# Performance work log

Measured on AMD Instinct MI355X. Metric: run time of the kernel, lower is better.

Reference implementation:

```python
import jax, jax.numpy as jnp
import numpy as np
from jax import ops as jops

N = 20000          # nodes
E = 320000         # edges
IN_DIM = 16        # input_dim_features_extractor
HID = 64           # hidden_dim_features_extractor
HEADS = 4          # n_attention_heads
LAYERS = 2         # n_layers_features_extractor
NEG_SLOPE = 0.2    # DGL EGATConv leaky_relu slope


def setup_inputs() -> dict:
    key = jax.random.key(0)
    ks = jax.random.split(key, 16)
    s = lambda *sh: 1.0 / np.sqrt(sh[-2] if len(sh) >= 2 else sh[-1])
    inp = {
        "node_feat": jax.random.normal(ks[0], (N, IN_DIM), jnp.float32),
        "edge_feat": jax.random.normal(ks[1], (E, HID), jnp.float32),
        "src": jax.random.randint(ks[2], (E,), 0, N, jnp.int32),
        "dst": jax.random.randint(ks[3], (E,), 0, N, jnp.int32),
        # features_embedder (MLP n_layers=1 -> single Linear IN_DIM->HID)
        "W_embed": jax.random.normal(ks[4], (IN_DIM, HID), jnp.float32) * s(IN_DIM, HID),
        "b_embed": jnp.zeros((HID,), jnp.float32),
        # per-layer EGATConv params (stacked over layer dim)
        "W_ni": jax.random.normal(ks[5], (LAYERS, HID, HEADS * HID), jnp.float32) * s(HID, 1),
        "W_nj": jax.random.normal(ks[6], (LAYERS, HID, HEADS * HID), jnp.float32) * s(HID, 1),
        "W_fij": jax.random.normal(ks[7], (LAYERS, HID, HEADS * HID), jnp.float32) * s(HID, 1),
        "b_att": jnp.zeros((LAYERS, HEADS * HID), jnp.float32),
        "attn": jax.random.normal(ks[8], (LAYERS, HEADS, HID), jnp.float32) * s(HID),
        "W_node": jax.random.normal(ks[9], (LAYERS, HID, HEADS * HID), jnp.float32) * s(HID, 1),
        # per-layer MLP (n_layers=1 -> Linear HEADS*HID -> HID)
        "W_mlp": jax.random.normal(ks[10], (LAYERS, HEADS * HID, HID), jnp.float32) * s(HEADS * HID, 1),
        "b_mlp": jnp.zeros((LAYERS, HID), jnp.float32),
    }
    return inp


def _egat(h, f, src, dst, W_ni, W_nj, W_fij, b, attn, W_node):
    """DGL EGATConv: edge-feature attention + softmax-weighted aggregation."""
    # per-edge attention features: u_add_v + edge proj + bias
    f_ni = h @ W_ni                         # (N, H*D)
    f_nj = h @ W_nj                         # (N, H*D)
    f_fij = f @ W_fij                       # (E, H*D)
    f_out = f_ni[src] + f_nj[dst] + f_fij + b
    f_out = jax.nn.leaky_relu(f_out, NEG_SLOPE).reshape(E, HEADS, HID)
    e = jnp.einsum("ehd,hd->eh", f_out, attn)            # (E, H) logits
    # edge softmax over incoming edges of each dst node (numerically stable)
    m = jops.segment_max(e, dst, num_segments=N)          # (N, H)
    a = jnp.exp(e - m[dst])
    z = jops.segment_sum(a, dst, num_segments=N)          # (N, H)
    a = a / z[dst]
    # weighted message aggregation
    hn = (h @ W_node).reshape(N, HEADS, HID)
    msg = hn[src] * a[:, :, None]                         # (E, H, D)
    out = jops.segment_sum(msg, dst, num_segments=N)      # (N, H, D)
    return out


def reference(node_feat, edge_feat, src, dst, W_embed, b_embed,
              W_ni, W_nj, W_fij, b_att, attn, W_node, W_mlp, b_mlp):
    features_list = [node_feat]                 # layer_pooling='all'
    features = node_feat @ W_embed + b_embed    # features_embedder
    features_list.append(features)
    for L in range(LAYERS):
        h = _egat(features, edge_feat, src, dst,
                  W_ni[L], W_nj[L], W_fij[L], b_att[L], attn[L], W_node[L])
        new = h.reshape(N, HEADS * HID) @ W_mlp[L] + b_mlp[L]
        features = new + features               # residual
        features_list.append(features)
    return jnp.concatenate(features_list, axis=-1)   # (N, 16 + 3*64)
```

## Files before the change

kernel.cpp:

```cpp
#include <hip/hip_runtime.h>
#include <math.h>

#define NN 20000
#define NE 320000
#define IN_DIM 16
#define HID 64
#define HEADS 4
#define HD 256
#define OUTW 208
#define NEG 0.2f

typedef unsigned short u16;
typedef unsigned int u32;
typedef __attribute__((ext_vector_type(8))) short bf16x8;
typedef __attribute__((ext_vector_type(8))) unsigned short u16x8;
typedef __attribute__((ext_vector_type(4))) float f32x4;

__device__ __forceinline__ float b2f(u16 u) {
  union { u32 i; float f; } c; c.i = ((u32)u) << 16; return c.f;
}
__device__ __forceinline__ u16 f2b(float f) {
  union { float f; u32 i; } c; c.f = f;
  u32 r = (c.i + 0x7FFFu + ((c.i >> 16) & 1u)) >> 16;
  return (u16)r;
}

__global__ void k_embed_count(const float* __restrict__ nf, const float* __restrict__ We,
                              const float* __restrict__ be, float* __restrict__ feat,
                              float* __restrict__ out, const int* __restrict__ dst,
                              int* __restrict__ counts) {
  int bid = blockIdx.x;
  const int EB = (NN * 64) / 256;
  if (bid < EB) {
    int tid = bid * 256 + threadIdx.x;
    int n = tid >> 6, c = tid & 63;
    float acc = be[c];
#pragma unroll
    for (int k = 0; k < IN_DIM; ++k)
      acc += nf[n * IN_DIM + k] * We[k * HID + c];
    feat[n * HID + c] = acc;
    out[n * OUTW + 16 + c] = acc;
    if (c < IN_DIM) out[n * OUTW + c] = nf[n * IN_DIM + c];
  } else {
    int e = (bid - EB) * 256 + threadIdx.x;
    if (e < NE) atomicAdd(&counts[dst[e]], 1);
  }
}

__global__ void k_scan(const int* __restrict__ counts, int* __restrict__ rowptr,
                       int* __restrict__ cursor) {
  __shared__ int wsum[16];
  const int PT = 20;
  int t = threadIdx.x;
  int lane = t & 63, wid = t >> 6;
  int base = t * PT;
  int c[PT];
  int tot = 0;
  if (t < 1000) {
#pragma unroll
    for (int i = 0; i < PT; ++i) {
      int v = counts[base + i];
      cursor[base + i] = 0;
      tot += v;
      c[i] = tot;
    }
  }
  int x = tot;
#pragma unroll
  for (int d = 1; d < 64; d <<= 1) {
    int y = __shfl_up(x, d);
    if (lane >= d) x += y;
  }
  int lexcl = x - tot;
  if (lane == 63) wsum[wid] = x;
  __syncthreads();
  if (wid == 0) {
    int wv = (lane < 16) ? wsum[lane] : 0;
#pragma unroll
    for (int d = 1; d < 16; d <<= 1) {
      int y = __shfl_up(wv, d);
      if (lane >= d) wv += y;
    }
    if (lane < 16) wsum[lane] = wv;
  }
  __syncthreads();
  int woff = (wid == 0) ? 0 : wsum[wid - 1];
  int offset = woff + lexcl;
  if (t == 0) rowptr[0] = 0;
  if (t < 1000) {
#pragma unroll
    for (int i = 0; i < PT; ++i) rowptr[base + i + 1] = offset + c[i];
  }
}

__global__ void k_scatter(const int* __restrict__ dst, const int* __restrict__ src,
                          const int* __restrict__ rowptr, int* __restrict__ cursor,
                          int* __restrict__ srcp, int* __restrict__ dstp,
                          int* __restrict__ pos_of) {
  int e = blockIdx.x * blockDim.x + threadIdx.x;
  if (e >= NE) return;
  int d = dst[e];
  int pos = rowptr[d] + atomicAdd(&cursor[d], 1);
  srcp[pos] = src[e];
  dstp[pos] = d;
  pos_of[e] = pos;
}

__global__ void k_permute_prepw(const float* __restrict__ ef, const int* __restrict__ pos_of,
                                u16* __restrict__ efbp, const float* __restrict__ Wf,
                                u16* __restrict__ Wt0, u16* __restrict__ Wt1) {
  int bid = blockIdx.x;
  const int PB = (NE * 16) / 256;
  if (bid < PB) {
    int t = bid * 256 + threadIdx.x;
    int e = t >> 4, c = (t & 15) * 4;
    int slot = pos_of[e];
    float4 v = *reinterpret_cast<const float4*>(&ef[(size_t)e * HID + c]);
    ushort4 o;
    o.x = f2b(v.x); o.y = f2b(v.y); o.z = f2b(v.z); o.w = f2b(v.w);
    *reinterpret_cast<ushort4*>(&efbp[(size_t)slot * HID + c]) = o;
  } else {
    int r = (bid - PB) * 256 + threadIdx.x;
    int Lw = r >> 14;
    int idx = r & 16383;
    int nn2 = idx >> 6, kk2 = idx & 63;
    u16* WtL = Lw ? Wt1 : Wt0;
    WtL[nn2 * HID + kk2] = f2b(Wf[(size_t)Lw * HID * HD + kk2 * HD + nn2]);
  }
}

__global__ __launch_bounds__(256) void k_nodeproj(
    const float* __restrict__ feat, const float* __restrict__ Wni,
    const float* __restrict__ Wnj, const float* __restrict__ Wnd,
    const float* __restrict__ batt, u16* __restrict__ fni,
    u16* __restrict__ fnj, u16* __restrict__ hn) {
  __shared__ float hs[8 * HID];
  int n0 = blockIdx.x * 8;
  int c = threadIdx.x;
  for (int i = threadIdx.x; i < 8 * HID; i += 256)
    hs[i] = feat[(size_t)(n0 + (i >> 6)) * HID + (i & 63)];
  __syncthreads();
  float aI[8] = {0}, aJ[8] = {0}, aN[8] = {0};
  for (int k = 0; k < HID; ++k) {
    float wi = Wni[k * HD + c], wj = Wnj[k * HD + c], wn = Wnd[k * HD + c];
#pragma unroll
    for (int t = 0; t < 8; ++t) {
      float x = hs[t * HID + k];
      aI[t] += x * wi; aJ[t] += x * wj; aN[t] += x * wn;
    }
  }
  float b = batt[c];
#pragma unroll
  for (int t = 0; t < 8; ++t) {
    int n = n0 + t;
    fni[(size_t)n * HD + c] = f2b(aI[t] + b);
    fnj[(size_t)n * HD + c] = f2b(aJ[t]);
    hn[(size_t)n * HD + c]  = f2b(aN[t]);
  }
}

__global__ __launch_bounds__(256) void k_edgelogits(
    const u16* __restrict__ efbp, const int* __restrict__ srcp,
    const int* __restrict__ dstp, const u16* __restrict__ fni,
    const u16* __restrict__ fnj, const u16* __restrict__ Wt,
    const float* __restrict__ attnL, float* __restrict__ elog) {
  __shared__ float gb[HEADS][16][68];
  int h = threadIdx.x >> 6;
  int l = threadIdx.x & 63;
  int q = l >> 4;
  int n = l & 15;
  bf16x8 bfr[4][2];
#pragma unroll
  for (int nt = 0; nt < 4; ++nt)
#pragma unroll
    for (int kk = 0; kk < 2; ++kk)
      bfr[nt][kk] = *reinterpret_cast<const bf16x8*>(
          &Wt[(h * 64 + nt * 16 + n) * HID + kk * 32 + q * 8]);
  float at[4];
#pragma unroll
  for (int nt = 0; nt < 4; ++nt) at[nt] = attnL[h * 64 + nt * 16 + n];

#define COMMIT(av, bv)                                                \
  {                                                                   \
    _Pragma("unroll")                                                 \
    for (int p = 0; p < 4; ++p) {                                     \
      float4 g;                                                       \
      g.x = b2f(av[p].x) + b2f(bv[p].x);                              \
      g.y = b2f(av[p].y) + b2f(bv[p].y);                              \
      g.z = b2f(av[p].z) + b2f(bv[p].z);                              \
      g.w = b2f(av[p].w) + b2f(bv[p].w);                              \
      *reinterpret_cast<float4*>(&gb[h][p * 4 + q][4 * n]) = g;       \
    }                                                                 \
  }

#define TILEMMA(aa0, aa1, ibase)                                                  \
  {                                                                               \
    float sumr[4] = {0.f, 0.f, 0.f, 0.f};                                         \
    _Pragma("unroll")                                                             \
    for (int nt = 0; nt < 4; ++nt) {                                              \
      f32x4 acc = {0.f, 0.f, 0.f, 0.f};                                           \
      acc = __builtin_amdgcn_mfma_f32_16x16x32_bf16(aa0, bfr[nt][0], acc, 0, 0, 0); \
      acc = __builtin_amdgcn_mfma_f32_16x16x32_bf16(aa1, bfr[nt][1], acc, 0, 0, 0); \
      _Pragma("unroll")                                                           \
      for (int r = 0; r < 4; ++r) {                                               \
        float v = acc[r] + gb[h][q * 4 + r][nt * 16 + n];                         \
        v = v > 0.f ? v : NEG * v;                                                \
        sumr[r] += v * at[nt];                                                    \
      }                                                                           \
    }                                                                             \
    _Pragma("unroll")                                                             \
    for (int r = 0; r < 4; ++r) {                                                 \
      float v = sumr[r];                                                          \
      v += __shfl_xor(v, 1);                                                      \
      v += __shfl_xor(v, 2);                                                      \
      v += __shfl_xor(v, 4);                                                      \
      v += __shfl_xor(v, 8);                                                      \
      sumr[r] = v;                                                                \
    }                                                                             \
    if (n == 0) {                                                                 \
      float4 o_;                                                                  \
      o_.x = sumr[0]; o_.y = sumr[1]; o_.z = sumr[2]; o_.w = sumr[3];             \
      *reinterpret_cast<float4*>(&elog[(size_t)h * NE + (ibase) + q * 4]) = o_;   \
    }                                                                             \
  }

  const int NT2 = NE / 32;
  const int G = gridDim.x;
  int swz = (blockIdx.x & 7) * (G >> 3) + (blockIdx.x >> 3);
  for (int pg = swz; pg < NT2; pg += G) {
    int i0 = pg * 32;
    int i1 = i0 + 16;
    bf16x8 a00 = *reinterpret_cast<const bf16x8*>(&efbp[(size_t)(i0 + n) * HID + q * 8]);
    bf16x8 a01 = *reinterpret_cast<const bf16x8*>(&efbp[(size_t)(i0 + n) * HID + 32 + q * 8]);
    ushort4 av0[4], bv0[4];
#pragma unroll
    for (int p = 0; p < 4; ++p) {
      int i = i0 + p * 4 + q;
      int s = srcp[i], d = dstp[i];
      av0[p] = *reinterpret_cast<const ushort4*>(&fni[(size_t)s * HD + h * 64 + 4 * n]);
      bv0[p] = *reinterpret_cast<const ushort4*>(&fnj[(size_t)d * HD + h * 64 + 4 * n]);
    }
    bf16x8 a10 = *reinterpret_cast<const bf16x8*>(&efbp[(size_t)(i1 + n) * HID + q * 8]);
    bf16x8 a11 = *reinterpret_cast<const bf16x8*>(&efbp[(size_t)(i1 + n) * HID + 32 + q * 8]);
    ushort4 av1[4], bv1[4];
#pragma unroll
    for (int p = 0; p < 4; ++p) {
      int i = i1 + p * 4 + q;
      int s = srcp[i], d = dstp[i];
      av1[p] = *reinterpret_cast<const ushort4*>(&fni[(size_t)s * HD + h * 64 + 4 * n]);
      bv1[p] = *reinterpret_cast<const ushort4*>(&fnj[(size_t)d * HD + h * 64 + 4 * n]);
    }
    COMMIT(av0, bv0);
    TILEMMA(a00, a01, i0);
    COMMIT(av1, bv1);
    TILEMMA(a10, a11, i1);
  }
#undef COMMIT
#undef TILEMMA
}

__global__ __launch_bounds__(256) void k_agg_mlp(
    const int* __restrict__ rowptr, const int* __restrict__ srcp,
    const float* __restrict__ elog, const u16* __restrict__ hn,
    const float* __restrict__ Wm, const float* __restrict__ bm,
    float* __restrict__ feat, float* __restrict__ out, int outoff) {
  __shared__ float as_[16 * HD];
  int j = threadIdx.x & 63;
  int wid = threadIdx.x >> 6;
  int half = j >> 5;
  int lo = j & 31;
  int hA = (j >> 3) & 3;
  int u = (j & 7) + 8 * half;
  const float* er = elog + (size_t)hA * NE;
  int n0 = blockIdx.x * 16;
#pragma unroll 1
  for (int t4 = 0; t4 < 4; ++t4) {
    int n = n0 + wid * 4 + t4;
    int s0 = rowptr[n], s1 = rowptr[n + 1];
    float m = -1e30f;
    for (int i = s0 + u; i < s1; i += 16) m = fmaxf(m, er[i]);
    m = fmaxf(m, __shfl_xor(m, 1));
    m = fmaxf(m, __shfl_xor(m, 2));
    m = fmaxf(m, __shfl_xor(m, 4));
    m = fmaxf(m, __shfl_xor(m, 32));
    float z = 0.f;
    for (int i = s0 + u; i < s1; i += 16) z += __expf(er[i] - m);
    z += __shfl_xor(z, 1);
    z += __shfl_xor(z, 2);
    z += __shfl_xor(z, 4);
    z += __shfl_xor(z, 32);
    float invz = (z > 0.f) ? 1.0f / z : 0.f;
    float a8[8] = {0.f, 0.f, 0.f, 0.f, 0.f, 0.f, 0.f, 0.f};
    int i = s0;
    for (; i + 8 <= s1; i += 8) {
      int sv[8]; float wv[8];
#pragma unroll
      for (int t = 0; t < 8; ++t) sv[t] = srcp[i + t];
#pragma unroll
      for (int t = 0; t < 8; ++t) wv[t] = __expf(er[i + t] - m) * invz;
      u16x8 vv[4];
#pragma unroll
      for (int g = 0; g < 4; ++g)
        vv[g] = *reinterpret_cast<const u16x8*>(&hn[(size_t)sv[2 * g + half] * HD + 8 * lo]);
#pragma unroll
      for (int g = 0; g < 4; ++g) {
        float w = wv[2 * g + half];
#pragma unroll
        for (int e = 0; e < 8; ++e) a8[e] += b2f(vv[g][e]) * w;
      }
    }
    for (; i + 2 <= s1; i += 2) {
      int s = srcp[i + half];
      float w = __expf(er[i + half] - m) * invz;
      u16x8 v = *reinterpret_cast<const u16x8*>(&hn[(size_t)s * HD + 8 * lo]);
#pragma unroll
      for (int e = 0; e < 8; ++e) a8[e] += b2f(v[e]) * w;
    }
    if (i < s1) {
      int s = srcp[i];
      float w = half ? 0.f : (__expf(er[i] - m) * invz);
      u16x8 v = *reinterpret_cast<const u16x8*>(&hn[(size_t)s * HD + 8 * lo]);
#pragma unroll
      for (int e = 0; e < 8; ++e) a8[e] += b2f(v[e]) * w;
    }
#pragma unroll
    for (int e = 0; e < 8; ++e) a8[e] += __shfl_xor(a8[e], 32);
    if (j < 32) {
      int row = wid * 4 + t4;
      float4 o0, o1;
      o0.x = a8[0]; o0.y = a8[1]; o0.z = a8[2]; o0.w = a8[3];
      o1.x = a8[4]; o1.y = a8[5]; o1.z = a8[6]; o1.w = a8[7];
      *reinterpret_cast<float4*>(&as_[row * HD + 8 * lo]) = o0;
      *reinterpret_cast<float4*>(&as_[row * HD + 8 * lo + 4]) = o1;
    }
  }
  __syncthreads();
  int c = threadIdx.x & 63;
  int g = threadIdx.x >> 6;
  float acc[4] = {0.f, 0.f, 0.f, 0.f};
  for (int k = 0; k < HD; ++k) {
    float wv = Wm[k * HID + c];
#pragma unroll
    for (int t = 0; t < 4; ++t)
      acc[t] += as_[(g * 4 + t) * HD + k] * wv;
  }
  float b = bm[c];
#pragma unroll
  for (int t = 0; t < 4; ++t) {
    int n = n0 + g * 4 + t;
    float v = acc[t] + b + feat[n * HID + c];
    feat[n * HID + c] = v;
    out[n * OUTW + outoff + c] = v;
  }
}

extern "C" void kernel_launch(void* const* d_in, const int* in_sizes, int n_in,
                              void* d_out, int out_size, void* d_ws, size_t ws_size,
                              hipStream_t stream) {
  const float* node_feat = (const float*)d_in[0];
  const float* edge_feat = (const float*)d_in[1];
  const int*   src       = (const int*)d_in[2];
  const int*   dst       = (const int*)d_in[3];
  const float* W_embed   = (const float*)d_in[4];
  const float* b_embed   = (const float*)d_in[5];
  const float* W_ni      = (const float*)d_in[6];
  const float* W_nj      = (const float*)d_in[7];
  const float* W_fij     = (const float*)d_in[8];
  const float* b_att     = (const float*)d_in[9];
  const float* attn      = (const float*)d_in[10];
  const float* W_node    = (const float*)d_in[11];
  const float* W_mlp     = (const float*)d_in[12];
  const float* b_mlp     = (const float*)d_in[13];
  float* out = (float*)d_out;

  float* ws   = (float*)d_ws;
  float* feat = ws;
  u16*  fni   = (u16*)(feat + (size_t)NN * HID);
  u16*  fnj   = fni + (size_t)NN * HD;
  u16*  hn    = fnj + (size_t)NN * HD;
  u16*  efbp  = hn + (size_t)NN * HD;
  u16*  Wt0   = efbp + (size_t)NE * HID;
  u16*  Wt1   = Wt0 + (size_t)HD * HID;
  float* elog = (float*)(Wt1 + (size_t)HD * HID);
  int* counts = (int*)(elog + (size_t)NE * HEADS);
  int* rowptr = counts + NN;
  int* cursor = rowptr + NN + 1;
  int* srcp   = cursor + NN;
  int* dstp   = srcp + NE;
  int* pos_of = dstp + NE;

  hipMemsetAsync(counts, 0, sizeof(int) * NN, stream);

  k_embed_count<<<(NN * 64) / 256 + NE / 256, 256, 0, stream>>>(
      node_feat, W_embed, b_embed, feat, out, dst, counts);
  k_scan<<<1, 1024, 0, stream>>>(counts, rowptr, cursor);
  k_scatter<<<NE / 256, 256, 0, stream>>>(dst, src, rowptr, cursor, srcp, dstp, pos_of);
  k_permute_prepw<<<(NE * 16) / 256 + 128, 256, 0, stream>>>(
      edge_feat, pos_of, efbp, W_fij, Wt0, Wt1);

  for (int L = 0; L < 2; ++L) {
    const float* WniL = W_ni + (size_t)L * HID * HD;
    const float* WnjL = W_nj + (size_t)L * HID * HD;
    const float* WndL = W_node + (size_t)L * HID * HD;
    const float* battL = b_att + (size_t)L * HD;
    const float* attnL = attn + (size_t)L * HEADS * HID;
    const float* WmL  = W_mlp + (size_t)L * HD * HID;
    const float* bmL  = b_mlp + (size_t)L * HID;
    u16* WtL = L ? Wt1 : Wt0;

    k_nodeproj<<<NN / 8, 256, 0, stream>>>(feat, WniL, WnjL, WndL, battL, fni, fnj, hn);
    k_edgelogits<<<2048, 256, 0, stream>>>(efbp, srcp, dstp, fni, fnj, WtL, attnL, elog);
    k_agg_mlp<<<NN / 16, 256, 0, stream>>>(rowptr, srcp, elog, hn, WmL, bmL,
                                           feat, out, 80 + L * 64);
  }
}
```

Measured before the change: 469.5 us.

## Fuse node projection into embed and layer-0 aggregation kernels

The standalone node-projection kernel is removed. For layer 0 the projection runs inside the embed/count kernel, and for layer 1 it runs as the tail of the layer-0 aggregation+MLP kernel, reusing the freshly computed features from shared memory. This removes two kernel launches and a global re-read of the features. hn is double-buffered (hnA/hnB) so the layer-1 projection does not overwrite the hn values that other blocks are still reading during layer-0 aggregation. Each fused block now handles 16 nodes instead of 8, which halves the number of projection blocks and lengthens the per-block tail. That may lower occupancy in these kernels.

Result: no change. 467.1 us (-0.5%).

```diff
diff --git a/kernel.cpp b/kernel.cpp
--- a/kernel.cpp
+++ b/kernel.cpp
@@ -25,22 +25,56 @@
   return (u16)r;
 }
 
-__global__ void k_embed_count(const float* __restrict__ nf, const float* __restrict__ We,
-                              const float* __restrict__ be, float* __restrict__ feat,
-                              float* __restrict__ out, const int* __restrict__ dst,
-                              int* __restrict__ counts) {
+__global__ __launch_bounds__(256) void k_embed_count_proj(
+    const float* __restrict__ nf, const float* __restrict__ We,
+    const float* __restrict__ be, const float* __restrict__ Wni,
+    const float* __restrict__ Wnj, const float* __restrict__ Wnd,
+    const float* __restrict__ batt, float* __restrict__ feat,
+    float* __restrict__ out, const int* __restrict__ dst,
+    int* __restrict__ counts, u16* __restrict__ fni,
+    u16* __restrict__ fnj, u16* __restrict__ hn) {
   int bid = blockIdx.x;
-  const int EB = (NN * 64) / 256;
+  const int EB = NN / 16;
   if (bid < EB) {
-    int tid = bid * 256 + threadIdx.x;
-    int n = tid >> 6, c = tid & 63;
-    float acc = be[c];
-#pragma unroll
-    for (int k = 0; k < IN_DIM; ++k)
-      acc += nf[n * IN_DIM + k] * We[k * HID + c];
-    feat[n * HID + c] = acc;
-    out[n * OUTW + 16 + c] = acc;
-    if (c < IN_DIM) out[n * OUTW + c] = nf[n * IN_DIM + c];
+    __shared__ float fs[16 * HID];
+    int n0 = bid * 16;
+    int c = threadIdx.x & 63;
+    int g = threadIdx.x >> 6;
+#pragma unroll
+    for (int t = 0; t < 4; ++t) {
+      int r = g * 4 + t;
+      int n = n0 + r;
+      float acc = be[c];
+#pragma unroll
+      for (int k = 0; k < IN_DIM; ++k)
+        acc += nf[n * IN_DIM + k] * We[k * HID + c];
+      fs[r * HID + c] = acc;
+      feat[(size_t)n * HID + c] = acc;
+      out[(size_t)n * OUTW + 16 + c] = acc;
+      if (c < IN_DIM) out[(size_t)n * OUTW + c] = nf[n * IN_DIM + c];
+    }
+    __syncthreads();
+    int cc = threadIdx.x;
+    float b = batt[cc];
+#pragma unroll 1
+    for (int h8 = 0; h8 < 2; ++h8) {
+      float aI[8] = {0}, aJ[8] = {0}, aN[8] = {0};
+      for (int k = 0; k < HID; ++k) {
+        float wi = Wni[k * HD + cc], wj = Wnj[k * HD + cc], wn = Wnd[k * HD + cc];
+#pragma unroll
+        for (int t = 0; t < 8; ++t) {
+          float x = fs[(h8 * 8 + t) * HID + k];
+          aI[t] += x * wi; aJ[t] += x * wj; aN[t] += x * wn;
+        }
+      }
+#pragma unroll
+      for (int t = 0; t < 8; ++t) {
+        int n = n0 + h8 * 8 + t;
+        fni[(size_t)n * HD + cc] = f2b(aI[t] + b);
+        fnj[(size_t)n * HD + cc] = f2b(aJ[t]);
+        hn[(size_t)n * HD + cc]  = f2b(aN[t]);
+      }
+    }
   } else {
     int e = (bid - EB) * 256 + threadIdx.x;
     if (e < NE) atomicAdd(&counts[dst[e]], 1);
@@ -126,36 +160,6 @@
     int nn2 = idx >> 6, kk2 = idx & 63;
     u16* WtL = Lw ? Wt1 : Wt0;
     WtL[nn2 * HID + kk2] = f2b(Wf[(size_t)Lw * HID * HD + kk2 * HD + nn2]);
-  }
-}
-
-__global__ __launch_bounds__(256) void k_nodeproj(
-    const float* __restrict__ feat, const float* __restrict__ Wni,
-    const float* __restrict__ Wnj, const float* __restrict__ Wnd,
-    const float* __restrict__ batt, u16* __restrict__ fni,
-    u16* __restrict__ fnj, u16* __restrict__ hn) {
-  __shared__ float hs[8 * HID];
-  int n0 = blockIdx.x * 8;
-  int c = threadIdx.x;
-  for (int i = threadIdx.x; i < 8 * HID; i += 256)
-    hs[i] = feat[(size_t)(n0 + (i >> 6)) * HID + (i & 63)];
-  __syncthreads();
-  float aI[8] = {0}, aJ[8] = {0}, aN[8] = {0};
-  for (int k = 0; k < HID; ++k) {
-    float wi = Wni[k * HD + c], wj = Wnj[k * HD + c], wn = Wnd[k * HD + c];
-#pragma unroll
-    for (int t = 0; t < 8; ++t) {
-      float x = hs[t * HID + k];
-      aI[t] += x * wi; aJ[t] += x * wj; aN[t] += x * wn;
-    }
-  }
-  float b = batt[c];
-#pragma unroll
-  for (int t = 0; t < 8; ++t) {
-    int n = n0 + t;
-    fni[(size_t)n * HD + c] = f2b(aI[t] + b);
-    fnj[(size_t)n * HD + c] = f2b(aJ[t]);
-    hn[(size_t)n * HD + c]  = f2b(aN[t]);
   }
 }
 
@@ -354,6 +358,131 @@
   }
 }
 
+__global__ __launch_bounds__(256) void k_agg_mlp_proj(
+    const int* __restrict__ rowptr, const int* __restrict__ srcp,
+    const float* __restrict__ elog, const u16* __restrict__ hn_in,
+    const float* __restrict__ Wm, const float* __restrict__ bm,
+    float* __restrict__ feat, float* __restrict__ out, int outoff,
+    const float* __restrict__ Wni, const float* __restrict__ Wnj,
+    const float* __restrict__ Wnd, const float* __restrict__ batt,
+    u16* __restrict__ fni, u16* __restrict__ fnj, u16* __restrict__ hn_out) {
+  __shared__ float as_[16 * HD];
+  __shared__ float fs[16 * HID];
+  int j = threadIdx.x & 63;
+  int wid = threadIdx.x >> 6;
+  int half = j >> 5;
+  int lo = j & 31;
+  int hA = (j >> 3) & 3;
+  int u = (j & 7) + 8 * half;
+  const float* er = elog + (size_t)hA * NE;
+  int n0 = blockIdx.x * 16;
+#pragma unroll 1
+  for (int t4 = 0; t4 < 4; ++t4) {
+    int n = n0 + wid * 4 + t4;
+    int s0 = rowptr[n], s1 = rowptr[n + 1];
+    float m = -1e30f;
+    for (int i = s0 + u; i < s1; i += 16) m = fmaxf(m, er[i]);
+    m = fmaxf(m, __shfl_xor(m, 1));
+    m = fmaxf(m, __shfl_xor(m, 2));
+    m = fmaxf(m, __shfl_xor(m, 4));
+    m = fmaxf(m, __shfl_xor(m, 32));
+    float z = 0.f;
+    for (int i = s0 + u; i < s1; i += 16) z += __expf(er[i] - m);
+    z += __shfl_xor(z, 1);
+    z += __shfl_xor(z, 2);
+    z += __shfl_xor(z, 4);
+    z += __shfl_xor(z, 32);
+    float invz = (z > 0.f) ? 1.0f / z : 0.f;
+    float a8[8] = {0.f, 0.f, 0.f, 0.f, 0.f, 0.f, 0.f, 0.f};
+    int i = s0;
+    for (; i + 8 <= s1; i += 8) {
+      int sv[8]; float wv[8];
+#pragma unroll
+      for (int t = 0; t < 8; ++t) sv[t] = srcp[i + t];
+#pragma unroll
+      for (int t = 0; t < 8; ++t) wv[t] = __expf(er[i + t] - m) * invz;
+      u16x8 vv[4];
+#pragma unroll
+      for (int g = 0; g < 4; ++g)
+        vv[g] = *reinterpret_cast<const u16x8*>(&hn_in[(size_t)sv[2 * g + half] * HD + 8 * lo]);
+#pragma unroll
+      for (int g = 0; g < 4; ++g) {
+        float w = wv[2 * g + half];
+#pragma unroll
+        for (int e = 0; e < 8; ++e) a8[e] += b2f(vv[g][e]) * w;
+      }
+    }
+    for (; i + 2 <= s1; i += 2) {
+      int s = srcp[i + half];
+      float w = __expf(er[i + half] - m) * invz;
+      u16x8 v = *reinterpret_cast<const u16x8*>(&hn_in[(size_t)s * HD + 8 * lo]);
+#pragma unroll
+      for (int e = 0; e < 8; ++e) a8[e] += b2f(v[e]) * w;
+    }
+    if (i < s1) {
+      int s = srcp[i];
+      float w = half ? 0.f : (__expf(er[i] - m) * invz);
+      u16x8 v = *reinterpret_cast<const u16x8*>(&hn_in[(size_t)s * HD + 8 * lo]);
+#pragma unroll
+      for (int e = 0; e < 8; ++e) a8[e] += b2f(v[e]) * w;
+    }
+#pragma unroll
+    for (int e = 0; e < 8; ++e) a8[e] += __shfl_xor(a8[e], 32);
+    if (j < 32) {
+      int row = wid * 4 + t4;
+      float4 o0, o1;
+      o0.x = a8[0]; o0.y = a8[1]; o0.z = a8[2]; o0.w = a8[3];
+      o1.x = a8[4]; o1.y = a8[5]; o1.z = a8[6]; o1.w = a8[7];
+      *reinterpret_cast<float4*>(&as_[row * HD + 8 * lo]) = o0;
+      *reinterpret_cast<float4*>(&as_[row * HD + 8 * lo + 4]) = o1;
+    }
+  }
+  __syncthreads();
+  {
+    int c = threadIdx.x & 63;
+    int g = threadIdx.x >> 6;
+    float acc[4] = {0.f, 0.f, 0.f, 0.f};
+    for (int k = 0; k < HD; ++k) {
+      float wv = Wm[k * HID + c];
+#pragma unroll
+      for (int t = 0; t < 4; ++t)
+        acc[t] += as_[(g * 4 + t) * HD + k] * wv;
+    }
+    float b = bm[c];
+#pragma unroll
+    for (int t = 0; t < 4; ++t) {
+      int r = g * 4 + t;
+      int n = n0 + r;
+      float v = acc[t] + b + feat[n * HID + c];
+      feat[n * HID + c] = v;
+      fs[r * HID + c] = v;
+      out[(size_t)n * OUTW + outoff + c] = v;
+    }
+  }
+  __syncthreads();
+  int cc = threadIdx.x;
+  float b2 = batt[cc];
+#pragma unroll 1
+  for (int h8 = 0; h8 < 2; ++h8) {
+    float aI[8] = {0}, aJ[8] = {0}, aN[8] = {0};
+    for (int k = 0; k < HID; ++k) {
+      float wi = Wni[k * HD + cc], wj = Wnj[k * HD + cc], wn = Wnd[k * HD + cc];
+#pragma unroll
+      for (int t = 0; t < 8; ++t) {
+        float x = fs[(h8 * 8 + t) * HID + k];
+        aI[t] += x * wi; aJ[t] += x * wj; aN[t] += x * wn;
+      }
+    }
+#pragma unroll
+    for (int t = 0; t < 8; ++t) {
+      int n = n0 + h8 * 8 + t;
+      fni[(size_t)n * HD + cc] = f2b(aI[t] + b2);
+      fnj[(size_t)n * HD + cc] = f2b(aJ[t]);
+      hn_out[(size_t)n * HD + cc] = f2b(aN[t]);
+    }
+  }
+}
+
 extern "C" void kernel_launch(void* const* d_in, const int* in_sizes, int n_in,
                               void* d_out, int out_size, void* d_ws, size_t ws_size,
                               hipStream_t stream) {
@@ -377,8 +506,9 @@
   float* feat = ws;
   u16*  fni   = (u16*)(feat + (size_t)NN * HID);
   u16*  fnj   = fni + (size_t)NN * HD;
-  u16*  hn    = fnj + (size_t)NN * HD;
-  u16*  efbp  = hn + (size_t)NN * HD;
+  u16*  hnA   = fnj + (size_t)NN * HD;
+  u16*  hnB   = hnA + (size_t)NN * HD;
+  u16*  efbp  = hnB + (size_t)NN * HD;
   u16*  Wt0   = efbp + (size_t)NE * HID;
   u16*  Wt1   = Wt0 + (size_t)HD * HID;
   float* elog = (float*)(Wt1 + (size_t)HD * HID);
@@ -391,26 +521,24 @@
 
   hipMemsetAsync(counts, 0, sizeof(int) * NN, stream);
 
-  k_embed_count<<<(NN * 64) / 256 + NE / 256, 256, 0, stream>>>(
-      node_feat, W_embed, b_embed, feat, out, dst, counts);
+  k_embed_count_proj<<<NN / 16 + NE / 256, 256, 0, stream>>>(
+      node_feat, W_embed, b_embed, W_ni, W_nj, W_node, b_att,
+      feat, out, dst, counts, fni, fnj, hnA);
   k_scan<<<1, 1024, 0, stream>>>(counts, rowptr, cursor);
   k_scatter<<<NE / 256, 256, 0, stream>>>(dst, src, rowptr, cursor, srcp, dstp, pos_of);
   k_permute_prepw<<<(NE * 16) / 256 + 128, 256, 0, stream>>>(
       edge_feat, pos_of, efbp, W_fij, Wt0, Wt1);
 
-  for (int L = 0; L < 2; ++L) {
-    const float* WniL = W_ni + (size_t)L * HID * HD;
-    const float* WnjL = W_nj + (size_t)L * HID * HD;
-    const float* WndL = W_node + (size_t)L * HID * HD;
-    const float* battL = b_att + (size_t)L * HD;
-    const float* attnL = attn + (size_t)L * HEADS * HID;
-    const float* WmL  = W_mlp + (size_t)L * HD * HID;
-    const float* bmL  = b_mlp + (size_t)L * HID;
-    u16* WtL = L ? Wt1 : Wt0;
-
-    k_nodeproj<<<NN / 8, 256, 0, stream>>>(feat, WniL, WnjL, WndL, battL, fni, fnj, hn);
-    k_edgelogits<<<2048, 256, 0, stream>>>(efbp, srcp, dstp, fni, fnj, WtL, attnL, elog);
-    k_agg_mlp<<<NN / 16, 256, 0, stream>>>(rowptr, srcp, elog, hn, WmL, bmL,
-                                           feat, out, 80 + L * 64);
-  }
-}
+  k_edgelogits<<<2048, 256, 0, stream>>>(efbp, srcp, dstp, fni, fnj, Wt0,
+                                         attn, elog);
+  k_agg_mlp_proj<<<NN / 16, 256, 0, stream>>>(
+      rowptr, srcp, elog, hnA, W_mlp, b_mlp, feat, out, 80,
+      W_ni + (size_t)HID * HD, W_nj + (size_t)HID * HD, W_node + (size_t)HID * HD,
+      b_att + HD, fni, fnj, hnB);
+
+  k_edgelogits<<<2048, 256, 0, stream>>>(efbp, srcp, dstp, fni, fnj, Wt1,
+                                         attn + HEADS * HID, elog);
+  k_agg_mlp<<<NN / 16, 256, 0, stream>>>(rowptr, srcp, elog, hnB,
+                                         W_mlp + (size_t)HD * HID, b_mlp + HID,
+                                         feat, out, 144);
+}
```
